# Optimization experiments

Measured on AMD Instinct MI355X. Metric: run time of the kernel, lower is better.

Reference implementation:

```python
import jax, jax.numpy as jnp
import numpy as np

N_NODES = 100000
N_EDGES = 1600000
D = 64
H = 128
EPS = 0.0  # learn_eps=False


def setup_inputs() -> dict:
    key = jax.random.key(0)
    k1, k2, k3, k4 = jax.random.split(key, 4)
    x = jax.random.normal(k1, (N_NODES, D), dtype=jnp.float32)
    edge_index = jax.random.randint(k2, (2, N_EDGES), 0, N_NODES, dtype=jnp.int64)
    W1 = jax.random.normal(k3, (D, H), dtype=jnp.float32) * (1.0 / np.sqrt(D))
    b1 = jnp.zeros((H,), dtype=jnp.float32)
    W2 = jax.random.normal(k4, (H, D), dtype=jnp.float32) * (1.0 / np.sqrt(H))
    b2 = jnp.zeros((D,), dtype=jnp.float32)
    return {"x": x, "edge_index": edge_index, "W1": W1, "b1": b1, "W2": W2, "b2": b2}


def reference(x, edge_index, W1, b1, W2, b2):
    src, dst = edge_index[0], edge_index[1]
    # gather neighbor features and scatter-add to destination nodes
    agg = jax.ops.segment_sum(x[src], dst, num_segments=N_NODES)  # [N, D]
    out = agg + (1.0 + EPS) * x
    # GIN MLP: Linear -> ReLU -> Linear
    h = jax.nn.relu(out @ W1 + b1)
    return h @ W2 + b2
```

## Files before the change

kernel.cpp:

```cpp
#include <hip/hip_runtime.h>

#define N_NODES 100000
#define N_EDGES 1600000
#define D 64
#define H 128
#define SCAN_BS 512
#define SCAN_NBLK ((N_NODES + SCAN_BS - 1) / SCAN_BS)

#define NB 1563
#define NCHUNK 256
#define EPC (N_EDGES / NCHUNK)
#define BCAP 2560
#define OVF_CAP 4096

#define MFMA_GRID 768
#define SH_STRIDE 132
#define SH16_ST 136

typedef __attribute__((ext_vector_type(8))) short short8;
typedef __attribute__((ext_vector_type(4))) float floatx4;
typedef __attribute__((ext_vector_type(4))) unsigned short ushort4_t;
typedef __attribute__((ext_vector_type(8))) unsigned short ushort8_t;

__device__ __forceinline__ unsigned short f2bf(float f) {
    unsigned u = __builtin_bit_cast(unsigned, f);
    u += 0x7FFFu + ((u >> 16) & 1u);
    return (unsigned short)(u >> 16);
}
__device__ __forceinline__ float bf2f(unsigned short u) {
    unsigned v = ((unsigned)u) << 16;
    return __builtin_bit_cast(float, v);
}

__global__ __launch_bounds__(256) void k_zero(int* __restrict__ p, int n) {
    int i = blockIdx.x * 256 + threadIdx.x;
    if (i < n) p[i] = 0;
}

__global__ __launch_bounds__(256) void k_pre(const float4* __restrict__ x4,
                                             ushort4_t* __restrict__ y, int n4,
                                             const int* __restrict__ dst,
                                             int* __restrict__ M2,
                                             int* __restrict__ ovfn,
                                             const float* __restrict__ W1,
                                             const float* __restrict__ W2,
                                             unsigned short* __restrict__ gW1b,
                                             unsigned short* __restrict__ gW2b) {
    __shared__ int hist[NB];
    int t = threadIdx.x, blk = blockIdx.x;
    if (blk < NCHUNK) {
        int c = blk;
        if (c == 0 && t == 0) ovfn[0] = 0;
        for (int i = t; i < NB; i += 256) hist[i] = 0;
        __syncthreads();
        const int* dp = dst + c * EPC;
        for (int i = t; i < EPC; i += 256) atomicAdd(&hist[dp[i] >> 6], 1);
        __syncthreads();
        int* mp = M2 + c * NB;
        for (int i = t; i < NB; i += 256) mp[i] = hist[i];
    } else if (blk == NCHUNK) {
        for (int q = t; q < 8192; q += 256) {
            int j = q & 7, l = (q >> 3) & 63, f = q >> 9;
            int nt = f & 7, kt = f >> 3;
            int k = kt * 32 + ((l >> 4) << 3) + j;
            int n = nt * 16 + (l & 15);
            gW1b[q] = f2bf(W1[k * H + n]);
        }
    } else if (blk == NCHUNK + 1) {
        for (int q = t; q < 8192; q += 256) {
            int j = q & 7, l = (q >> 3) & 63, f = q >> 9;
            int nt = f & 3, kt = f >> 2;
            int k = kt * 32 + ((l >> 4) << 3) + j;
            int n = nt * 16 + (l & 15);
            gW2b[q] = f2bf(W2[k * D + n]);
        }
    } else {
        int cb = blk - NCHUNK - 2;
        int nconv = gridDim.x - NCHUNK - 2;
        for (int i = cb * 256 + t; i < n4; i += nconv * 256) {
            float4 v = x4[i];
            ushort4_t o;
            o[0] = f2bf(v.x); o[1] = f2bf(v.y); o[2] = f2bf(v.z); o[3] = f2bf(v.w);
            y[i] = o;
        }
    }
}

__global__ __launch_bounds__(256) void k_colscan(int* __restrict__ M2,
                                                 int* __restrict__ colsum) {
    int b = blockIdx.x * 256 + threadIdx.x;
    if (b >= NB) return;
    int run = 0;
    for (int c = 0; c < NCHUNK; c++) {
        int v = M2[c * NB + b];
        M2[c * NB + b] = run;
        run += v;
    }
    colsum[b] = run;
}

__global__ __launch_bounds__(512) void k_bscan(const int* __restrict__ colsum,
                                               int* __restrict__ bends) {
    __shared__ int part[512];
    int t = threadIdx.x;
    int i0 = t * 4;
    int v0 = (i0 + 0 < NB) ? colsum[i0 + 0] : 0;
    int v1 = (i0 + 1 < NB) ? colsum[i0 + 1] : 0;
    int v2 = (i0 + 2 < NB) ? colsum[i0 + 2] : 0;
    int v3 = (i0 + 3 < NB) ? colsum[i0 + 3] : 0;
    int r0 = v0, r1 = r0 + v1, r2 = r1 + v2, r3 = r2 + v3;
    part[t] = r3;
    __syncthreads();
    for (int off = 1; off < 512; off <<= 1) {
        int u = (t >= off) ? part[t - off] : 0;
        __syncthreads();
        part[t] += u;
        __syncthreads();
    }
    int base = (t > 0) ? part[t - 1] : 0;
    if (i0 + 0 < NB) bends[i0 + 0] = base + r0;
    if (i0 + 1 < NB) bends[i0 + 1] = base + r1;
    if (i0 + 2 < NB) bends[i0 + 2] = base + r2;
    if (i0 + 3 < NB) bends[i0 + 3] = base + r3;
}

__global__ __launch_bounds__(256) void k_part(const int* __restrict__ src,
                                              const int* __restrict__ dst,
                                              const int* __restrict__ M2,
                                              const int* __restrict__ bends,
                                              int* __restrict__ ebuf) {
    __shared__ int cur[NB];
    int t = threadIdx.x, c = blockIdx.x;
    const int* mp = M2 + c * NB;
    for (int i = t; i < NB; i += 256)
        cur[i] = ((i > 0) ? bends[i - 1] : 0) + mp[i];
    __syncthreads();
    const int* sp = src + c * EPC;
    const int* dp = dst + c * EPC;
    for (int i = t; i < EPC; i += 256) {
        int d = dp[i], s = sp[i];
        int p = atomicAdd(&cur[d >> 6], 1);
        ebuf[p] = s | ((d & 63) << 17);
    }
}

__global__ __launch_bounds__(256) void k_bagg4(const float* __restrict__ x,
                                               const unsigned short* __restrict__ x16,
                                               const int* __restrict__ ebuf,
                                               const int* __restrict__ bends,
                                               int* __restrict__ ovfn,
                                               int* __restrict__ ovf,
                                               unsigned short* __restrict__ o16) {
    __shared__ int scur[64];
    __shared__ int snd[64];
    __shared__ int slist[BCAP];
    int t = threadIdx.x, b = blockIdx.x;
    int estart = (b > 0) ? bends[b - 1] : 0;
    int ne = bends[b] - estart;
    const int* ep = ebuf + estart;

    if (t < 64) scur[t] = 0;
    __syncthreads();
    for (int i = t; i < ne; i += 256) atomicAdd(&scur[ep[i] >> 17], 1);
    __syncthreads();
    if (t < 64) {
        int v = scur[t], s = v;
#pragma unroll
        for (int off = 1; off < 64; off <<= 1) {
            int u = __shfl_up(s, off, 64);
            if (t >= off) s += u;
        }
        snd[t] = s;
        scur[t] = s - v;
    }
    __syncthreads();
    for (int i = t; i < ne; i += 256) {
        int v = ep[i];
        int p = atomicAdd(&scur[v >> 17], 1);
        if (p < BCAP) {
            slist[p] = v & 0x1FFFF;
        } else {
            int o = atomicAdd(ovfn, 1);
            if (o < OVF_CAP) { ovf[2 * o] = b * 64 + (v >> 17); ovf[2 * o + 1] = v & 0x1FFFF; }
        }
    }
    __syncthreads();

    int g = t >> 3;
    int l8 = t & 7;
#pragma unroll
    for (int k = 0; k < 2; k++) {
        int dlow = g * 2 + k;
        int node = b * 64 + dlow;
        int s0 = (dlow > 0) ? snd[dlow - 1] : 0;
        int e1 = snd[dlow];
        if (s0 > BCAP) s0 = BCAP;
        if (e1 > BCAP) e1 = BCAP;
        float accA[8], accB[8];
#pragma unroll
        for (int j = 0; j < 8; j++) { accA[j] = 0.f; accB[j] = 0.f; }
        int i = s0;
        for (; i + 4 <= e1; i += 4) {
            int sA = slist[i], sB = slist[i + 1], sC = slist[i + 2], sD = slist[i + 3];
            ushort8_t uA = *(const ushort8_t*)&x16[(size_t)sA * D + l8 * 8];
            ushort8_t uB = *(const ushort8_t*)&x16[(size_t)sB * D + l8 * 8];
            ushort8_t uC = *(const ushort8_t*)&x16[(size_t)sC * D + l8 * 8];
            ushort8_t uD = *(const ushort8_t*)&x16[(size_t)sD * D + l8 * 8];
#pragma unroll
            for (int j = 0; j < 8; j++) accA[j] += bf2f(uA[j]);
#pragma unroll
            for (int j = 0; j < 8; j++) accB[j] += bf2f(uB[j]);
#pragma unroll
            for (int j = 0; j < 8; j++) accA[j] += bf2f(uC[j]);
#pragma unroll
            for (int j = 0; j < 8; j++) accB[j] += bf2f(uD[j]);
        }
        for (; i < e1; i++) {
            int sA = slist[i];
            ushort8_t uA = *(const ushort8_t*)&x16[(size_t)sA * D + l8 * 8];
#pragma unroll
            for (int j = 0; j < 8; j++) accA[j] += bf2f(uA[j]);
        }
        if (node < N_NODES) {
            const float* xp = x + (size_t)node * D + l8 * 8;
            float4 x0 = *(const float4*)xp;
            float4 x1 = *(const float4*)(xp + 4);
            ushort8_t o;
            o[0] = f2bf(accA[0] + accB[0] + x0.x);
            o[1] = f2bf(accA[1] + accB[1] + x0.y);
            o[2] = f2bf(accA[2] + accB[2] + x0.z);
            o[3] = f2bf(accA[3] + accB[3] + x0.w);
            o[4] = f2bf(accA[4] + accB[4] + x1.x);
            o[5] = f2bf(accA[5] + accB[5] + x1.y);
            o[6] = f2bf(accA[6] + accB[6] + x1.z);
            o[7] = f2bf(accA[7] + accB[7] + x1.w);
            *(ushort8_t*)&o16[(size_t)node * D + l8 * 8] = o;
        }
    }
}

__global__ __launch_bounds__(64) void k_ovf(const int* __restrict__ ovfn,
                                            const int* __restrict__ ovf,
                                            const float* __restrict__ x,
                                            unsigned short* __restrict__ o16) {
    int n = *ovfn;
    if (n > OVF_CAP) n = OVF_CAP;
    int f = threadIdx.x;
    for (int idx = 0; idx < n; idx++) {
        int d = ovf[2 * idx], s = ovf[2 * idx + 1];
        unsigned short* p = &o16[(size_t)d * D + f];
        *p = f2bf(bf2f(*p) + x[(size_t)s * D + f]);
    }
}

__global__ __launch_bounds__(256) void k_mlp16(const unsigned short* __restrict__ in16,
                                               float* __restrict__ outp,
                                               const unsigned short* __restrict__ gW1b,
                                               const unsigned short* __restrict__ gW2b,
                                               const float* __restrict__ b1,
                                               const float* __restrict__ b2) {
    __shared__ unsigned short sW1b[8192];
    __shared__ unsigned short sW2b[8192];
    __shared__ unsigned short sh16[4][16 * SH16_ST];
    __shared__ float sb1[H];
    __shared__ float sb2[D];

    int t = threadIdx.x;
    for (int q = t; q < 1024; q += 256) {
        *(short8*)&sW1b[q * 8] = *(const short8*)&gW1b[q * 8];
        *(short8*)&sW2b[q * 8] = *(const short8*)&gW2b[q * 8];
    }
    if (t < H) sb1[t] = b1[t];
    if (t >= H && t < H + D) sb2[t - H] = b2[t - H];
    __syncthreads();

    int w = t >> 6, l = t & 63;
    int m = l & 15, q4 = l >> 4;
    unsigned short* shw = sh16[w];

    const int NT16 = N_NODES / 16;
    const int WAVES = MFMA_GRID * 4;
    const int ITERS = (NT16 + WAVES - 1) / WAVES;

    for (int it = 0; it < ITERS; ++it) {
        int tl = it * WAVES + blockIdx.x * 4 + w;
        bool valid = tl < NT16;
        int nbase = tl * 16;

        if (valid) {
            const unsigned short* xr = in16 + (size_t)(nbase + m) * D + q4 * 8;
            short8 A0 = *(const short8*)(xr);
            short8 A1 = *(const short8*)(xr + 32);

#pragma unroll
            for (int nt = 0; nt < 8; nt++) {
                float bv = sb1[nt * 16 + m];
                floatx4 acc = {bv, bv, bv, bv};
                short8 B0 = *(const short8*)&sW1b[(0 * 8 + nt) * 512 + l * 8];
                short8 B1 = *(const short8*)&sW1b[(1 * 8 + nt) * 512 + l * 8];
                acc = __builtin_amdgcn_mfma_f32_16x16x32_bf16(A0, B0, acc, 0, 0, 0);
                acc = __builtin_amdgcn_mfma_f32_16x16x32_bf16(A1, B1, acc, 0, 0, 0);
#pragma unroll
                for (int r = 0; r < 4; r++)
                    shw[(q4 * 4 + r) * SH16_ST + nt * 16 + m] = f2bf(fmaxf(acc[r], 0.f));
            }
        }
        __syncthreads();

        if (valid) {
            short8 Ah[4];
#pragma unroll
            for (int kt = 0; kt < 4; kt++)
                Ah[kt] = *(const short8*)&shw[m * SH16_ST + kt * 32 + q4 * 8];
#pragma unroll
            for (int nt = 0; nt < 4; nt++) {
                float bv = sb2[nt * 16 + m];
                floatx4 acc = {bv, bv, bv, bv};
#pragma unroll
                for (int kt = 0; kt < 4; kt++) {
                    short8 B = *(const short8*)&sW2b[(kt * 4 + nt) * 512 + l * 8];
                    acc = __builtin_amdgcn_mfma_f32_16x16x32_bf16(Ah[kt], B, acc, 0, 0, 0);
                }
#pragma unroll
                for (int r = 0; r < 4; r++)
                    outp[(size_t)(nbase + q4 * 4 + r) * D + nt * 16 + m] = acc[r];
            }
        }
        __syncthreads();
    }
}

__global__ __launch_bounds__(256) void k_mlp_f32(float* __restrict__ io,
                                                 const float* __restrict__ W1,
                                                 const float* __restrict__ b1,
                                                 const float* __restrict__ W2,
                                                 const float* __restrict__ b2) {
    __shared__ unsigned short sW1b[8192];
    __shared__ unsigned short sW2b[8192];
    __shared__ float sh[4][16 * SH_STRIDE];
    __shared__ float sb1[H];
    __shared__ float sb2[D];

    int t = threadIdx.x;

    for (int q = t; q < 8192; q += 256) {
        int j = q & 7, l = (q >> 3) & 63, f = q >> 9;
        int nt = f & 7, kt = f >> 3;
        int k = kt * 32 + ((l >> 4) << 3) + j;
        int n = nt * 16 + (l & 15);
        sW1b[q] = f2bf(W1[k * H + n]);
    }
    for (int q = t; q < 8192; q += 256) {
        int j = q & 7, l = (q >> 3) & 63, f = q >> 9;
        int nt = f & 3, kt = f >> 2;
        int k = kt * 32 + ((l >> 4) << 3) + j;
        int n = nt * 16 + (l & 15);
        sW2b[q] = f2bf(W2[k * D + n]);
    }
    if (t < H) sb1[t] = b1[t];
    if (t >= H && t < H + D) sb2[t - H] = b2[t - H];
    __syncthreads();

    int w = t >> 6, l = t & 63;
    int m = l & 15, q4 = l >> 4;
    float* shw = sh[w];

    const int NT16 = N_NODES / 16;
    const int WAVES = 512 * 4;
    const int ITERS = (NT16 + WAVES - 1) / WAVES;

    for (int it = 0; it < ITERS; ++it) {
        int tl = it * WAVES + blockIdx.x * 4 + w;
        bool valid = tl < NT16;
        int nbase = tl * 16;

        if (valid) {
            const float* xr = io + (size_t)(nbase + m) * D + q4 * 8;
            float4 a0 = *(const float4*)(xr);
            float4 a1 = *(const float4*)(xr + 4);
            float4 c0 = *(const float4*)(xr + 32);
            float4 c1 = *(const float4*)(xr + 36);
            short8 A0, A1;
            A0[0] = f2bf(a0.x); A0[1] = f2bf(a0.y); A0[2] = f2bf(a0.z); A0[3] = f2bf(a0.w);
            A0[4] = f2bf(a1.x); A0[5] = f2bf(a1.y); A0[6] = f2bf(a1.z); A0[7] = f2bf(a1.w);
            A1[0] = f2bf(c0.x); A1[1] = f2bf(c0.y); A1[2] = f2bf(c0.z); A1[3] = f2bf(c0.w);
            A1[4] = f2bf(c1.x); A1[5] = f2bf(c1.y); A1[6] = f2bf(c1.z); A1[7] = f2bf(c1.w);

#pragma unroll
            for (int nt = 0; nt < 8; nt++) {
                float bv = sb1[nt * 16 + m];
                floatx4 acc = {bv, bv, bv, bv};
                short8 B0 = *(const short8*)&sW1b[(0 * 8 + nt) * 512 + l * 8];
                short8 B1 = *(const short8*)&sW1b[(1 * 8 + nt) * 512 + l * 8];
                acc = __builtin_amdgcn_mfma_f32_16x16x32_bf16(A0, B0, acc, 0, 0, 0);
                acc = __builtin_amdgcn_mfma_f32_16x16x32_bf16(A1, B1, acc, 0, 0, 0);
#pragma unroll
                for (int r = 0; r < 4; r++)
                    shw[(q4 * 4 + r) * SH_STRIDE + nt * 16 + m] = fmaxf(acc[r], 0.f);
            }
        }
        __syncthreads();

        if (valid) {
            short8 Ah[4];
#pragma unroll
            for (int kt = 0; kt < 4; kt++) {
                const float* hr = &shw[m * SH_STRIDE + kt * 32 + q4 * 8];
                float4 h0 = *(const float4*)(hr);
                float4 h1 = *(const float4*)(hr + 4);
                Ah[kt][0] = f2bf(h0.x); Ah[kt][1] = f2bf(h0.y);
                Ah[kt][2] = f2bf(h0.z); Ah[kt][3] = f2bf(h0.w);
                Ah[kt][4] = f2bf(h1.x); Ah[kt][5] = f2bf(h1.y);
                Ah[kt][6] = f2bf(h1.z); Ah[kt][7] = f2bf(h1.w);
            }
#pragma unroll
            for (int nt = 0; nt < 4; nt++) {
                float bv = sb2[nt * 16 + m];
                floatx4 acc = {bv, bv, bv, bv};
#pragma unroll
                for (int kt = 0; kt < 4; kt++) {
                    short8 B = *(const short8*)&sW2b[(kt * 4 + nt) * 512 + l * 8];
                    acc = __builtin_amdgcn_mfma_f32_16x16x32_bf16(Ah[kt], B, acc, 0, 0, 0);
                }
#pragma unroll
                for (int r = 0; r < 4; r++)
                    io[(size_t)(nbase + q4 * 4 + r) * D + nt * 16 + m] = acc[r];
            }
        }
        __syncthreads();
    }
}

__global__ __launch_bounds__(SCAN_BS) void k_scan1(const int* __restrict__ cnt,
                                                   int* __restrict__ ends,
                                                   int* __restrict__ bsum, int n) {
    __shared__ int s[SCAN_BS];
    int t = threadIdx.x, b = blockIdx.x;
    int id = b * SCAN_BS + t;
    s[t] = (id < n) ? cnt[id] : 0;
    __syncthreads();
    for (int off = 1; off < SCAN_BS; off <<= 1) {
        int u = (t >= off) ? s[t - off] : 0;
        __syncthreads();
        s[t] += u;
        __syncthreads();
    }
    if (id < n) ends[id] = s[t];
    if (t == SCAN_BS - 1) bsum[b] = s[t];
}

__global__ __launch_bounds__(256) void k_scan2(int* __restrict__ bsum, int nb) {
    __shared__ int s[256];
    int t = threadIdx.x;
    s[t] = (t < nb) ? bsum[t] : 0;
    __syncthreads();
    for (int off = 1; off < 256; off <<= 1) {
        int u = (t >= off) ? s[t - off] : 0;
        __syncthreads();
        s[t] += u;
        __syncthreads();
    }
    if (t < nb) bsum[t] = s[t];
}

__global__ __launch_bounds__(SCAN_BS) void k_scan3(int* __restrict__ ends,
                                                   const int* __restrict__ bsum, int n) {
    int t = threadIdx.x, b = blockIdx.x;
    int id = b * SCAN_BS + t;
    if (b > 0 && id < n) ends[id] += bsum[b - 1];
}

__global__ __launch_bounds__(256) void k_histpos(const int* __restrict__ dst,
                                                 int* __restrict__ cnt,
                                                 int* __restrict__ pos) {
    int e = blockIdx.x * 256 + threadIdx.x;
    if (e < N_EDGES) pos[e] = atomicAdd(&cnt[dst[e]], 1);
}

__global__ __launch_bounds__(256) void k_fill2(const int* __restrict__ src,
                                               const int* __restrict__ dst,
                                               const int* __restrict__ pos,
                                               const int* __restrict__ ends,
                                               int* __restrict__ csr) {
    int e = blockIdx.x * 256 + threadIdx.x;
    if (e >= N_EDGES) return;
    int d = dst[e];
    int start = (d > 0) ? ends[d - 1] : 0;
    csr[start + pos[e]] = src[e];
}

__global__ __launch_bounds__(256) void k_agg(const float* __restrict__ x,
                                             const int* __restrict__ csr,
                                             const int* __restrict__ ends,
                                             float* __restrict__ out) {
    int node = blockIdx.x * 4 + (threadIdx.x >> 6);
    if (node >= N_NODES) return;
    int f = threadIdx.x & 63;
    int start = (node > 0) ? ends[node - 1] : 0;
    int end = ends[node];
    float a0 = x[(size_t)node * D + f], a1 = 0.f, a2 = 0.f, a3 = 0.f;
    int e = start;
    for (; e + 4 <= end; e += 4) {
        int s0 = csr[e], s1 = csr[e + 1], s2 = csr[e + 2], s3 = csr[e + 3];
        a0 += x[(size_t)s0 * D + f];
        a1 += x[(size_t)s1 * D + f];
        a2 += x[(size_t)s2 * D + f];
        a3 += x[(size_t)s3 * D + f];
    }
    for (; e < end; e++) a0 += x[(size_t)csr[e] * D + f];
    out[(size_t)node * D + f] = (a0 + a1) + (a2 + a3);
}

__global__ __launch_bounds__(256) void k_init(const float4* __restrict__ x4,
                                              float4* __restrict__ agg4, int n4) {
    int i = blockIdx.x * 256 + threadIdx.x;
    if (i < n4) agg4[i] = x4[i];
}

__global__ __launch_bounds__(256) void k_scatter(const float4* __restrict__ x4,
                                                 const int* __restrict__ src,
                                                 const int* __restrict__ dst,
                                                 float* __restrict__ agg) {
    int gid = blockIdx.x * 256 + threadIdx.x;
    int e = gid >> 4;
    if (e >= N_EDGES) return;
    int c = gid & 15;
    float4 v = x4[src[e] * 16 + c];
    float* p = agg + (size_t)dst[e] * D + c * 4;
    atomicAdd(p + 0, v.x);
    atomicAdd(p + 1, v.y);
    atomicAdd(p + 2, v.z);
    atomicAdd(p + 3, v.w);
}

extern "C" void kernel_launch(void* const* d_in, const int* in_sizes, int n_in,
                              void* d_out, int out_size, void* d_ws, size_t ws_size,
                              hipStream_t stream) {
    const float* x  = (const float*)d_in[0];
    const int* eidx = (const int*)d_in[1];
    const float* W1 = (const float*)d_in[2];
    const float* b1 = (const float*)d_in[3];
    const float* W2 = (const float*)d_in[4];
    const float* b2 = (const float*)d_in[5];
    float* out      = (float*)d_out;

    const int* src = eidx;
    const int* dst = eidx + N_EDGES;

    int ge = (N_EDGES + 255) / 256;
    int n4 = N_NODES * D / 4;

    size_t need_A = (size_t)N_NODES * D * 2 * sizeof(unsigned short)
                  + (size_t)(N_EDGES + NCHUNK * NB + 2 * NB + 4 + 2 * OVF_CAP) * sizeof(int)
                  + (size_t)16384 * sizeof(unsigned short);
    size_t need_B = (size_t)(2 * N_NODES + 512 + 2 * N_EDGES) * sizeof(int);

    if (ws_size >= need_A) {
        unsigned short* x16 = (unsigned short*)d_ws;
        unsigned short* o16 = x16 + (size_t)N_NODES * D;
        int* ebuf   = (int*)(o16 + (size_t)N_NODES * D);
        int* M2     = ebuf + N_EDGES;
        int* colsum = M2 + NCHUNK * NB;
        int* bends  = colsum + NB;
        int* ovfn   = bends + NB;
        int* ovf    = ovfn + 4;
        unsigned short* gW1b = (unsigned short*)(ovf + 2 * OVF_CAP);
        unsigned short* gW2b = gW1b + 8192;

        k_pre<<<NCHUNK + 2 + 2048, 256, 0, stream>>>((const float4*)x, (ushort4_t*)x16, n4,
                                                     dst, M2, ovfn, W1, W2, gW1b, gW2b);
        k_colscan<<<(NB + 255) / 256, 256, 0, stream>>>(M2, colsum);
        k_bscan<<<1, 512, 0, stream>>>(colsum, bends);
        k_part<<<NCHUNK, 256, 0, stream>>>(src, dst, M2, bends, ebuf);
        k_bagg4<<<NB, 256, 0, stream>>>(x, x16, ebuf, bends, ovfn, ovf, o16);
        k_ovf<<<1, 64, 0, stream>>>(ovfn, ovf, x, o16);
        k_mlp16<<<MFMA_GRID, 256, 0, stream>>>(o16, out, gW1b, gW2b, b1, b2);
    } else if (ws_size >= need_B) {
        int* cnt  = (int*)d_ws;
        int* ends = cnt + N_NODES;
        int* bsum = ends + N_NODES;
        int* pos  = bsum + 512;
        int* csr  = pos + N_EDGES;

        k_zero<<<(N_NODES + 255) / 256, 256, 0, stream>>>(cnt, N_NODES);
        k_histpos<<<ge, 256, 0, stream>>>(dst, cnt, pos);
        k_scan1<<<SCAN_NBLK, SCAN_BS, 0, stream>>>(cnt, ends, bsum, N_NODES);
        k_scan2<<<1, 256, 0, stream>>>(bsum, SCAN_NBLK);
        k_scan3<<<SCAN_NBLK, SCAN_BS, 0, stream>>>(ends, bsum, N_NODES);
        k_fill2<<<ge, 256, 0, stream>>>(src, dst, pos, ends, csr);
        k_agg<<<(N_NODES + 3) / 4, 256, 0, stream>>>(x, csr, ends, out);
        k_mlp_f32<<<512, 256, 0, stream>>>(out, W1, b1, W2, b2);
    } else {
        k_init<<<(n4 + 255) / 256, 256, 0, stream>>>((const float4*)x, (float4*)out, n4);
        long long total = (long long)N_EDGES * 16;
        k_scatter<<<(int)((total + 255) / 256), 256, 0, stream>>>(
            (const float4*)x, src, dst, out);
        k_mlp_f32<<<512, 256, 0, stream>>>(out, W1, b1, W2, b2);
    }
}
```

Baseline: 176.9 us.

## Merge graph preprocessing into one cooperative kernel with global-atomic partitioning

Replaces the chunked histogram, column scan, block scan, partition and bucket-aggregate kernels with a single cooperative kernel that uses grid.sync between phases. It uses global atomics for a 32-node bucket histogram and partition cursors, and every block redundantly scans the bucket histogram in shared memory. Oversized buckets are handled by tiling the edge list instead of an overflow path. The goal is to remove several launches and the per-chunk count matrix. The cost is heavy global atomic contention, grid-wide barriers, and a partition order that is no longer deterministic.

```diff
diff --git a/kernel.cpp b/kernel.cpp
--- a/kernel.cpp
+++ b/kernel.cpp
@@ -1,4 +1,7 @@
 #include <hip/hip_runtime.h>
+#include <hip/hip_cooperative_groups.h>
+
+namespace cg = cooperative_groups;
 
 #define N_NODES 100000
 #define N_EDGES 1600000
@@ -7,11 +10,9 @@
 #define SCAN_BS 512
 #define SCAN_NBLK ((N_NODES + SCAN_BS - 1) / SCAN_BS)
 
-#define NB 1563
-#define NCHUNK 256
-#define EPC (N_EDGES / NCHUNK)
-#define BCAP 2560
-#define OVF_CAP 4096
+#define BK 32
+#define NB2 3125
+#define BCAP2 1536
 
 #define MFMA_GRID 768
 #define SH_STRIDE 132
@@ -32,33 +33,31 @@
     return __builtin_bit_cast(float, v);
 }
 
-__global__ __launch_bounds__(256) void k_zero(int* __restrict__ p, int n) {
-    int i = blockIdx.x * 256 + threadIdx.x;
-    if (i < n) p[i] = 0;
-}
-
-__global__ __launch_bounds__(256) void k_pre(const float4* __restrict__ x4,
-                                             ushort4_t* __restrict__ y, int n4,
-                                             const int* __restrict__ dst,
-                                             int* __restrict__ M2,
-                                             int* __restrict__ ovfn,
-                                             const float* __restrict__ W1,
-                                             const float* __restrict__ W2,
-                                             unsigned short* __restrict__ gW1b,
-                                             unsigned short* __restrict__ gW2b) {
-    __shared__ int hist[NB];
-    int t = threadIdx.x, blk = blockIdx.x;
-    if (blk < NCHUNK) {
-        int c = blk;
-        if (c == 0 && t == 0) ovfn[0] = 0;
-        for (int i = t; i < NB; i += 256) hist[i] = 0;
-        __syncthreads();
-        const int* dp = dst + c * EPC;
-        for (int i = t; i < EPC; i += 256) atomicAdd(&hist[dp[i] >> 6], 1);
-        __syncthreads();
-        int* mp = M2 + c * NB;
-        for (int i = t; i < NB; i += 256) mp[i] = hist[i];
-    } else if (blk == NCHUNK) {
+
+__device__ __forceinline__ void phase_pre(const float* x, unsigned short* x16,
+                                          const int* dst,
+                                          const float* W1, const float* W2,
+                                          unsigned short* gW1b,
+                                          unsigned short* gW2b,
+                                          int* bhist) {
+    int t = threadIdx.x;
+    int stride = gridDim.x * 256;
+    int start = blockIdx.x * 256 + t;
+
+    for (int i = start; i < N_EDGES; i += stride)
+        atomicAdd(&bhist[dst[i] >> 5], 1);
+
+    const float4* x4 = (const float4*)x;
+    ushort4_t* y = (ushort4_t*)x16;
+    const int n4 = N_NODES * D / 4;
+    for (int i = start; i < n4; i += stride) {
+        float4 v = x4[i];
+        ushort4_t o;
+        o[0] = f2bf(v.x); o[1] = f2bf(v.y); o[2] = f2bf(v.z); o[3] = f2bf(v.w);
+        y[i] = o;
+    }
+
+    if (blockIdx.x == 0) {
         for (int q = t; q < 8192; q += 256) {
             int j = q & 7, l = (q >> 3) & 63, f = q >> 9;
             int nt = f & 7, kt = f >> 3;
@@ -66,7 +65,7 @@
             int n = nt * 16 + (l & 15);
             gW1b[q] = f2bf(W1[k * H + n]);
         }
-    } else if (blk == NCHUNK + 1) {
+    } else if (blockIdx.x == 1) {
         for (int q = t; q < 8192; q += 256) {
             int j = q & 7, l = (q >> 3) & 63, f = q >> 9;
             int nt = f & 3, kt = f >> 2;
@@ -74,183 +73,187 @@
             int n = nt * 16 + (l & 15);
             gW2b[q] = f2bf(W2[k * D + n]);
         }
-    } else {
-        int cb = blk - NCHUNK - 2;
-        int nconv = gridDim.x - NCHUNK - 2;
-        for (int i = cb * 256 + t; i < n4; i += nconv * 256) {
-            float4 v = x4[i];
-            ushort4_t o;
-            o[0] = f2bf(v.x); o[1] = f2bf(v.y); o[2] = f2bf(v.z); o[3] = f2bf(v.w);
-            y[i] = o;
-        }
-    }
-}
-
-__global__ __launch_bounds__(256) void k_colscan(int* __restrict__ M2,
-                                                 int* __restrict__ colsum) {
-    int b = blockIdx.x * 256 + threadIdx.x;
-    if (b >= NB) return;
-    int run = 0;
-    for (int c = 0; c < NCHUNK; c++) {
-        int v = M2[c * NB + b];
-        M2[c * NB + b] = run;
-        run += v;
-    }
-    colsum[b] = run;
-}
-
-__global__ __launch_bounds__(512) void k_bscan(const int* __restrict__ colsum,
-                                               int* __restrict__ bends) {
-    __shared__ int part[512];
+    }
+}
+
+__device__ __forceinline__ void phase_scan(const int* bhist, int* sstart,
+                                           int* spart) {
     int t = threadIdx.x;
-    int i0 = t * 4;
-    int v0 = (i0 + 0 < NB) ? colsum[i0 + 0] : 0;
-    int v1 = (i0 + 1 < NB) ? colsum[i0 + 1] : 0;
-    int v2 = (i0 + 2 < NB) ? colsum[i0 + 2] : 0;
-    int v3 = (i0 + 3 < NB) ? colsum[i0 + 3] : 0;
-    int r0 = v0, r1 = r0 + v1, r2 = r1 + v2, r3 = r2 + v3;
-    part[t] = r3;
+    int base = t * 13;
+    int v[13];
+    int s = 0;
+#pragma unroll
+    for (int j = 0; j < 13; j++) {
+        int idx = base + j;
+        v[j] = (idx < NB2) ? bhist[idx] : 0;
+        s += v[j];
+    }
+    spart[t] = s;
     __syncthreads();
-    for (int off = 1; off < 512; off <<= 1) {
-        int u = (t >= off) ? part[t - off] : 0;
-        __syncthreads();
-        part[t] += u;
-        __syncthreads();
-    }
-    int base = (t > 0) ? part[t - 1] : 0;
-    if (i0 + 0 < NB) bends[i0 + 0] = base + r0;
-    if (i0 + 1 < NB) bends[i0 + 1] = base + r1;
-    if (i0 + 2 < NB) bends[i0 + 2] = base + r2;
-    if (i0 + 3 < NB) bends[i0 + 3] = base + r3;
-}
-
-__global__ __launch_bounds__(256) void k_part(const int* __restrict__ src,
-                                              const int* __restrict__ dst,
-                                              const int* __restrict__ M2,
-                                              const int* __restrict__ bends,
-                                              int* __restrict__ ebuf) {
-    __shared__ int cur[NB];
-    int t = threadIdx.x, c = blockIdx.x;
-    const int* mp = M2 + c * NB;
-    for (int i = t; i < NB; i += 256)
-        cur[i] = ((i > 0) ? bends[i - 1] : 0) + mp[i];
+    for (int off = 1; off < 256; off <<= 1) {
+        int u = (t >= off) ? spart[t - off] : 0;
+        __syncthreads();
+        spart[t] += u;
+        __syncthreads();
+    }
+    int run = (t > 0) ? spart[t - 1] : 0;
+#pragma unroll
+    for (int j = 0; j < 13; j++) {
+        int idx = base + j;
+        if (idx < NB2) sstart[idx] = run;
+        run += v[j];
+    }
+    if (t == 0) sstart[NB2] = N_EDGES;
     __syncthreads();
-    const int* sp = src + c * EPC;
-    const int* dp = dst + c * EPC;
-    for (int i = t; i < EPC; i += 256) {
-        int d = dp[i], s = sp[i];
-        int p = atomicAdd(&cur[d >> 6], 1);
-        ebuf[p] = s | ((d & 63) << 17);
-    }
-}
-
-__global__ __launch_bounds__(256) void k_bagg4(const float* __restrict__ x,
-                                               const unsigned short* __restrict__ x16,
-                                               const int* __restrict__ ebuf,
-                                               const int* __restrict__ bends,
-                                               int* __restrict__ ovfn,
-                                               int* __restrict__ ovf,
-                                               unsigned short* __restrict__ o16) {
-    __shared__ int scur[64];
-    __shared__ int snd[64];
-    __shared__ int slist[BCAP];
-    int t = threadIdx.x, b = blockIdx.x;
-    int estart = (b > 0) ? bends[b - 1] : 0;
-    int ne = bends[b] - estart;
-    const int* ep = ebuf + estart;
-
-    if (t < 64) scur[t] = 0;
-    __syncthreads();
-    for (int i = t; i < ne; i += 256) atomicAdd(&scur[ep[i] >> 17], 1);
-    __syncthreads();
-    if (t < 64) {
-        int v = scur[t], s = v;
-#pragma unroll
-        for (int off = 1; off < 64; off <<= 1) {
-            int u = __shfl_up(s, off, 64);
-            if (t >= off) s += u;
-        }
-        snd[t] = s;
-        scur[t] = s - v;
-    }
-    __syncthreads();
-    for (int i = t; i < ne; i += 256) {
-        int v = ep[i];
-        int p = atomicAdd(&scur[v >> 17], 1);
-        if (p < BCAP) {
-            slist[p] = v & 0x1FFFF;
-        } else {
-            int o = atomicAdd(ovfn, 1);
-            if (o < OVF_CAP) { ovf[2 * o] = b * 64 + (v >> 17); ovf[2 * o + 1] = v & 0x1FFFF; }
-        }
-    }
-    __syncthreads();
-
+}
+
+__device__ __forceinline__ void phase_part(const int* src, const int* dst,
+                                           const int* sstart, int* ccur,
+                                           int* ebuf) {
+    int t = threadIdx.x;
+    int stride = gridDim.x * 256;
+    for (int i = blockIdx.x * 256 + t; i < N_EDGES; i += stride) {
+        int d = dst[i], s = src[i];
+        int b = d >> 5;
+        int p = sstart[b] + atomicAdd(&ccur[b], 1);
+        ebuf[p] = s | ((d & 31) << 17);
+    }
+}
+
+__device__ __forceinline__ void phase_bagg(const float* x,
+                                           const unsigned short* x16,
+                                           const int* ebuf, const int* sstart,
+                                           int* scur, int* snd, int* slist,
+                                           unsigned short* o16) {
+    int t = threadIdx.x;
     int g = t >> 3;
     int l8 = t & 7;
-#pragma unroll
-    for (int k = 0; k < 2; k++) {
-        int dlow = g * 2 + k;
-        int node = b * 64 + dlow;
-        int s0 = (dlow > 0) ? snd[dlow - 1] : 0;
-        int e1 = snd[dlow];
-        if (s0 > BCAP) s0 = BCAP;
-        if (e1 > BCAP) e1 = BCAP;
+    for (int b = blockIdx.x; b < NB2; b += gridDim.x) {
+        int estart = sstart[b];
+        int ne = sstart[b + 1] - estart;
+        const int* ep = ebuf + estart;
         float accA[8], accB[8];
 #pragma unroll
         for (int j = 0; j < 8; j++) { accA[j] = 0.f; accB[j] = 0.f; }
-        int i = s0;
-        for (; i + 4 <= e1; i += 4) {
-            int sA = slist[i], sB = slist[i + 1], sC = slist[i + 2], sD = slist[i + 3];
-            ushort8_t uA = *(const ushort8_t*)&x16[(size_t)sA * D + l8 * 8];
-            ushort8_t uB = *(const ushort8_t*)&x16[(size_t)sB * D + l8 * 8];
-            ushort8_t uC = *(const ushort8_t*)&x16[(size_t)sC * D + l8 * 8];
-            ushort8_t uD = *(const ushort8_t*)&x16[(size_t)sD * D + l8 * 8];
-#pragma unroll
-            for (int j = 0; j < 8; j++) accA[j] += bf2f(uA[j]);
-#pragma unroll
-            for (int j = 0; j < 8; j++) accB[j] += bf2f(uB[j]);
-#pragma unroll
-            for (int j = 0; j < 8; j++) accA[j] += bf2f(uC[j]);
-#pragma unroll
-            for (int j = 0; j < 8; j++) accB[j] += bf2f(uD[j]);
-        }
-        for (; i < e1; i++) {
-            int sA = slist[i];
-            ushort8_t uA = *(const ushort8_t*)&x16[(size_t)sA * D + l8 * 8];
-#pragma unroll
-            for (int j = 0; j < 8; j++) accA[j] += bf2f(uA[j]);
-        }
-        if (node < N_NODES) {
-            const float* xp = x + (size_t)node * D + l8 * 8;
-            float4 x0 = *(const float4*)xp;
-            float4 x1 = *(const float4*)(xp + 4);
-            ushort8_t o;
-            o[0] = f2bf(accA[0] + accB[0] + x0.x);
-            o[1] = f2bf(accA[1] + accB[1] + x0.y);
-            o[2] = f2bf(accA[2] + accB[2] + x0.z);
-            o[3] = f2bf(accA[3] + accB[3] + x0.w);
-            o[4] = f2bf(accA[4] + accB[4] + x1.x);
-            o[5] = f2bf(accA[5] + accB[5] + x1.y);
-            o[6] = f2bf(accA[6] + accB[6] + x1.z);
-            o[7] = f2bf(accA[7] + accB[7] + x1.w);
-            *(ushort8_t*)&o16[(size_t)node * D + l8 * 8] = o;
-        }
-    }
-}
-
-__global__ __launch_bounds__(64) void k_ovf(const int* __restrict__ ovfn,
-                                            const int* __restrict__ ovf,
-                                            const float* __restrict__ x,
-                                            unsigned short* __restrict__ o16) {
-    int n = *ovfn;
-    if (n > OVF_CAP) n = OVF_CAP;
-    int f = threadIdx.x;
-    for (int idx = 0; idx < n; idx++) {
-        int d = ovf[2 * idx], s = ovf[2 * idx + 1];
-        unsigned short* p = &o16[(size_t)d * D + f];
-        *p = f2bf(bf2f(*p) + x[(size_t)s * D + f]);
-    }
+
+        int ntile = (ne + BCAP2 - 1) / BCAP2;
+        for (int T = 0; T < ntile; T++) {
+            int toff = T * BCAP2;
+            int tn = ne - toff;
+            if (tn > BCAP2) tn = BCAP2;
+            __syncthreads();
+            if (t < BK) scur[t] = 0;
+            __syncthreads();
+            for (int i = t; i < tn; i += 256)
+                atomicAdd(&scur[ep[toff + i] >> 17], 1);
+            __syncthreads();
+            if (t < BK) {
+                int v = scur[t], s = v;
+#pragma unroll
+                for (int off = 1; off < BK; off <<= 1) {
+                    int u = __shfl_up(s, off, 64);
+                    if (t >= off) s += u;
+                }
+                snd[t] = s;
+                scur[t] = s - v;
+            }
+            __syncthreads();
+            for (int i = t; i < tn; i += 256) {
+                int v = ep[toff + i];
+                int p = atomicAdd(&scur[v >> 17], 1);
+                slist[p] = v & 0x1FFFF;
+            }
+            __syncthreads();
+
+            int s0 = (g > 0) ? snd[g - 1] : 0;
+            int e1 = snd[g];
+            int i2 = s0;
+            for (; i2 + 4 <= e1; i2 += 4) {
+                int sA = slist[i2], sB = slist[i2 + 1];
+                int sC = slist[i2 + 2], sD = slist[i2 + 3];
+                ushort8_t uA = *(const ushort8_t*)&x16[(size_t)sA * D + l8 * 8];
+                ushort8_t uB = *(const ushort8_t*)&x16[(size_t)sB * D + l8 * 8];
+                ushort8_t uC = *(const ushort8_t*)&x16[(size_t)sC * D + l8 * 8];
+                ushort8_t uD = *(const ushort8_t*)&x16[(size_t)sD * D + l8 * 8];
+#pragma unroll
+                for (int j = 0; j < 8; j++) accA[j] += bf2f(uA[j]);
+#pragma unroll
+                for (int j = 0; j < 8; j++) accB[j] += bf2f(uB[j]);
+#pragma unroll
+                for (int j = 0; j < 8; j++) accA[j] += bf2f(uC[j]);
+#pragma unroll
+                for (int j = 0; j < 8; j++) accB[j] += bf2f(uD[j]);
+            }
+            for (; i2 < e1; i2++) {
+                ushort8_t uA =
+                    *(const ushort8_t*)&x16[(size_t)slist[i2] * D + l8 * 8];
+#pragma unroll
+                for (int j = 0; j < 8; j++) accA[j] += bf2f(uA[j]);
+            }
+        }
+
+        int node = b * BK + g;
+        const float* xp = x + (size_t)node * D + l8 * 8;
+        float4 x0 = *(const float4*)xp;
+        float4 x1 = *(const float4*)(xp + 4);
+        ushort8_t o;
+        o[0] = f2bf(accA[0] + accB[0] + x0.x);
+        o[1] = f2bf(accA[1] + accB[1] + x0.y);
+        o[2] = f2bf(accA[2] + accB[2] + x0.z);
+        o[3] = f2bf(accA[3] + accB[3] + x0.w);
+        o[4] = f2bf(accA[4] + accB[4] + x1.x);
+        o[5] = f2bf(accA[5] + accB[5] + x1.y);
+        o[6] = f2bf(accA[6] + accB[6] + x1.z);
+        o[7] = f2bf(accA[7] + accB[7] + x1.w);
+        *(ushort8_t*)&o16[(size_t)node * D + l8 * 8] = o;
+    }
+}
+
+__global__ __launch_bounds__(256) void k_graph(const float* x,
+                                               unsigned short* x16,
+                                               const int* src, const int* dst,
+                                               const float* W1,
+                                               const float* W2,
+                                               unsigned short* gW1b,
+                                               unsigned short* gW2b,
+                                               int* bhist, int* ccur,
+                                               int* ebuf,
+                                               unsigned short* o16) {
+    __shared__ int sstart[NB2 + 1];
+    __shared__ int sbuf[2 * BK + BCAP2];
+    cg::grid_group grid = cg::this_grid();
+
+    phase_pre(x, x16, dst, W1, W2, gW1b, gW2b, bhist);
+    grid.sync();
+    phase_scan(bhist, sstart, sbuf);
+    phase_part(src, dst, sstart, ccur, ebuf);
+    grid.sync();
+    phase_bagg(x, x16, ebuf, sstart, sbuf, sbuf + BK, sbuf + 2 * BK, o16);
+}
+
+__global__ __launch_bounds__(256) void k_p1(const float* x, unsigned short* x16,
+                                            const int* dst, const float* W1,
+                                            const float* W2,
+                                            unsigned short* gW1b,
+                                            unsigned short* gW2b, int* bhist) {
+    phase_pre(x, x16, dst, W1, W2, gW1b, gW2b, bhist);
+}
+__global__ __launch_bounds__(256) void k_p2(const int* src, const int* dst,
+                                            const int* bhist, int* ccur,
+                                            int* ebuf) {
+    __shared__ int sstart[NB2 + 1];
+    __shared__ int sbuf[2 * BK + BCAP2];
+    phase_scan(bhist, sstart, sbuf);
+    phase_part(src, dst, sstart, ccur, ebuf);
+}
+__global__ __launch_bounds__(256) void k_p3(const float* x,
+                                            const unsigned short* x16,
+                                            const int* ebuf, const int* bhist,
+                                            unsigned short* o16) {
+    __shared__ int sstart[NB2 + 1];
+    __shared__ int sbuf[2 * BK + BCAP2];
+    phase_scan(bhist, sstart, sbuf);
+    phase_bagg(x, x16, ebuf, sstart, sbuf, sbuf + BK, sbuf + 2 * BK, o16);
 }
 
 __global__ __launch_bounds__(256) void k_mlp16(const unsigned short* __restrict__ in16,
@@ -328,6 +331,11 @@
         }
         __syncthreads();
     }
+}
+
+__global__ __launch_bounds__(256) void k_zero(int* __restrict__ p, int n) {
+    int i = blockIdx.x * 256 + threadIdx.x;
+    if (i < n) p[i] = 0;
 }
 
 __global__ __launch_bounds__(256) void k_mlp_f32(float* __restrict__ io,
@@ -551,29 +559,47 @@
     int n4 = N_NODES * D / 4;
 
     size_t need_A = (size_t)N_NODES * D * 2 * sizeof(unsigned short)
-                  + (size_t)(N_EDGES + NCHUNK * NB + 2 * NB + 4 + 2 * OVF_CAP) * sizeof(int)
-                  + (size_t)16384 * sizeof(unsigned short);
+                  + (size_t)N_EDGES * sizeof(int)
+                  + (size_t)16384 * sizeof(unsigned short)
+                  + (size_t)2 * NB2 * sizeof(int);
     size_t need_B = (size_t)(2 * N_NODES + 512 + 2 * N_EDGES) * sizeof(int);
 
     if (ws_size >= need_A) {
         unsigned short* x16 = (unsigned short*)d_ws;
         unsigned short* o16 = x16 + (size_t)N_NODES * D;
         int* ebuf   = (int*)(o16 + (size_t)N_NODES * D);
-        int* M2     = ebuf + N_EDGES;
-        int* colsum = M2 + NCHUNK * NB;
-        int* bends  = colsum + NB;
-        int* ovfn   = bends + NB;
-        int* ovf    = ovfn + 4;
-        unsigned short* gW1b = (unsigned short*)(ovf + 2 * OVF_CAP);
+        unsigned short* gW1b = (unsigned short*)(ebuf + N_EDGES);
         unsigned short* gW2b = gW1b + 8192;
-
-        k_pre<<<NCHUNK + 2 + 2048, 256, 0, stream>>>((const float4*)x, (ushort4_t*)x16, n4,
-                                                     dst, M2, ovfn, W1, W2, gW1b, gW2b);
-        k_colscan<<<(NB + 255) / 256, 256, 0, stream>>>(M2, colsum);
-        k_bscan<<<1, 512, 0, stream>>>(colsum, bends);
-        k_part<<<NCHUNK, 256, 0, stream>>>(src, dst, M2, bends, ebuf);
-        k_bagg4<<<NB, 256, 0, stream>>>(x, x16, ebuf, bends, ovfn, ovf, o16);
-        k_ovf<<<1, 64, 0, stream>>>(ovfn, ovf, x, o16);
+        int* bhist  = (int*)(gW2b + 8192);
+        int* ccur   = bhist + NB2;
+
+        static int G = 0;
+        if (G == 0) {
+            int nb = 0;
+            if (hipOccupancyMaxActiveBlocksPerMultiprocessor(&nb, k_graph, 256, 0)
+                    != hipSuccess || nb < 1)
+                nb = 1;
+            long g = (long)nb * 256;
+            if (g > 1024) g = 1024;
+            if (g < 256) g = 256;
+            G = (int)g;
+        }
+
+        hipMemsetAsync(bhist, 0, 2 * NB2 * sizeof(int), stream);
+
+        const float* xa = x;
+        unsigned short* x16a = x16;
+        void* kargs[] = {(void*)&xa, (void*)&x16a, (void*)&src, (void*)&dst,
+                         (void*)&W1, (void*)&W2, (void*)&gW1b, (void*)&gW2b,
+                         (void*)&bhist, (void*)&ccur, (void*)&ebuf, (void*)&o16};
+        hipError_t ce = hipLaunchCooperativeKernel(k_graph, dim3(G), dim3(256),
+                                                   kargs, 0u, stream);
+        if (ce != hipSuccess) {
+            (void)hipGetLastError();
+            k_p1<<<1024, 256, 0, stream>>>(x, x16, dst, W1, W2, gW1b, gW2b, bhist);
+            k_p2<<<1024, 256, 0, stream>>>(src, dst, bhist, ccur, ebuf);
+            k_p3<<<1024, 256, 0, stream>>>(x, x16, ebuf, bhist, o16);
+        }
         k_mlp16<<<MFMA_GRID, 256, 0, stream>>>(o16, out, gW1b, gW2b, b1, b2);
     } else if (ws_size >= need_B) {
         int* cnt  = (int*)d_ws;
```

Result: slower. 622.5 us (+251.9%).

## Fold bucket scan into partition kernel and tile aggregation to drop overflow path

Applied to the files above, without the earlier changes.

The single-block bucket-end scan is recomputed redundantly inside every partition block, which removes one kernel launch. The overflow buffer and its serial fix-up kernel are replaced by processing each bucket's edges in tiles of BCAP, with accumulators kept in registers across tiles. The gather inner loop unroll drops from 4 to 2 loads per iteration across two register accumulator sets. The trade-offs are redundant scan work in every block, lower memory-level parallelism in the gather, and higher register pressure.

```diff
diff --git a/kernel.cpp b/kernel.cpp
--- a/kernel.cpp
+++ b/kernel.cpp
@@ -11,7 +11,6 @@
 #define NCHUNK 256
 #define EPC (N_EDGES / NCHUNK)
 #define BCAP 2560
-#define OVF_CAP 4096
 
 #define MFMA_GRID 768
 #define SH_STRIDE 132
@@ -32,16 +31,10 @@
     return __builtin_bit_cast(float, v);
 }
 
-__global__ __launch_bounds__(256) void k_zero(int* __restrict__ p, int n) {
-    int i = blockIdx.x * 256 + threadIdx.x;
-    if (i < n) p[i] = 0;
-}
-
 __global__ __launch_bounds__(256) void k_pre(const float4* __restrict__ x4,
                                              ushort4_t* __restrict__ y, int n4,
                                              const int* __restrict__ dst,
                                              int* __restrict__ M2,
-                                             int* __restrict__ ovfn,
                                              const float* __restrict__ W1,
                                              const float* __restrict__ W2,
                                              unsigned short* __restrict__ gW1b,
@@ -50,7 +43,6 @@
     int t = threadIdx.x, blk = blockIdx.x;
     if (blk < NCHUNK) {
         int c = blk;
-        if (c == 0 && t == 0) ovfn[0] = 0;
         for (int i = t; i < NB; i += 256) hist[i] = 0;
         __syncthreads();
         const int* dp = dst + c * EPC;
@@ -99,157 +91,168 @@
     colsum[b] = run;
 }
 
-__global__ __launch_bounds__(512) void k_bscan(const int* __restrict__ colsum,
-                                               int* __restrict__ bends) {
-    __shared__ int part[512];
-    int t = threadIdx.x;
-    int i0 = t * 4;
-    int v0 = (i0 + 0 < NB) ? colsum[i0 + 0] : 0;
-    int v1 = (i0 + 1 < NB) ? colsum[i0 + 1] : 0;
-    int v2 = (i0 + 2 < NB) ? colsum[i0 + 2] : 0;
-    int v3 = (i0 + 3 < NB) ? colsum[i0 + 3] : 0;
-    int r0 = v0, r1 = r0 + v1, r2 = r1 + v2, r3 = r2 + v3;
-    part[t] = r3;
+__global__ __launch_bounds__(256) void k_part2(const int* __restrict__ src,
+                                               const int* __restrict__ dst,
+                                               const int* __restrict__ M2,
+                                               const int* __restrict__ colsum,
+                                               int* __restrict__ ebuf,
+                                               int* __restrict__ gbends) {
+    __shared__ int cur[NB];
+    __shared__ int sbends[NB];
+    __shared__ int spart[256];
+    int t = threadIdx.x, c = blockIdx.x;
+
+    int base = t * 7;
+    int v[7];
+    int s = 0;
+#pragma unroll
+    for (int j = 0; j < 7; j++) {
+        int idx = base + j;
+        v[j] = (idx < NB) ? colsum[idx] : 0;
+        s += v[j];
+    }
+    spart[t] = s;
     __syncthreads();
-    for (int off = 1; off < 512; off <<= 1) {
-        int u = (t >= off) ? part[t - off] : 0;
-        __syncthreads();
-        part[t] += u;
-        __syncthreads();
-    }
-    int base = (t > 0) ? part[t - 1] : 0;
-    if (i0 + 0 < NB) bends[i0 + 0] = base + r0;
-    if (i0 + 1 < NB) bends[i0 + 1] = base + r1;
-    if (i0 + 2 < NB) bends[i0 + 2] = base + r2;
-    if (i0 + 3 < NB) bends[i0 + 3] = base + r3;
-}
-
-__global__ __launch_bounds__(256) void k_part(const int* __restrict__ src,
-                                              const int* __restrict__ dst,
-                                              const int* __restrict__ M2,
-                                              const int* __restrict__ bends,
-                                              int* __restrict__ ebuf) {
-    __shared__ int cur[NB];
-    int t = threadIdx.x, c = blockIdx.x;
+    for (int off = 1; off < 256; off <<= 1) {
+        int u = (t >= off) ? spart[t - off] : 0;
+        __syncthreads();
+        spart[t] += u;
+        __syncthreads();
+    }
+    int run = (t > 0) ? spart[t - 1] : 0;
+#pragma unroll
+    for (int j = 0; j < 7; j++) {
+        int idx = base + j;
+        run += v[j];
+        if (idx < NB) sbends[idx] = run;
+    }
+    __syncthreads();
+
     const int* mp = M2 + c * NB;
     for (int i = t; i < NB; i += 256)
-        cur[i] = ((i > 0) ? bends[i - 1] : 0) + mp[i];
+        cur[i] = ((i > 0) ? sbends[i - 1] : 0) + mp[i];
+    if (c == 0)
+        for (int i = t; i < NB; i += 256) gbends[i] = sbends[i];
     __syncthreads();
+
     const int* sp = src + c * EPC;
     const int* dp = dst + c * EPC;
     for (int i = t; i < EPC; i += 256) {
-        int d = dp[i], s = sp[i];
+        int d = dp[i], srcv = sp[i];
         int p = atomicAdd(&cur[d >> 6], 1);
-        ebuf[p] = s | ((d & 63) << 17);
-    }
-}
-
-__global__ __launch_bounds__(256) void k_bagg4(const float* __restrict__ x,
+        ebuf[p] = srcv | ((d & 63) << 17);
+    }
+}
+
+__global__ __launch_bounds__(256) void k_bagg5(const float* __restrict__ x,
                                                const unsigned short* __restrict__ x16,
                                                const int* __restrict__ ebuf,
-                                               const int* __restrict__ bends,
-                                               int* __restrict__ ovfn,
-                                               int* __restrict__ ovf,
+                                               const int* __restrict__ gbends,
                                                unsigned short* __restrict__ o16) {
     __shared__ int scur[64];
     __shared__ int snd[64];
     __shared__ int slist[BCAP];
     int t = threadIdx.x, b = blockIdx.x;
-    int estart = (b > 0) ? bends[b - 1] : 0;
-    int ne = bends[b] - estart;
+    int estart = (b > 0) ? gbends[b - 1] : 0;
+    int ne = gbends[b] - estart;
     const int* ep = ebuf + estart;
-
-    if (t < 64) scur[t] = 0;
-    __syncthreads();
-    for (int i = t; i < ne; i += 256) atomicAdd(&scur[ep[i] >> 17], 1);
-    __syncthreads();
-    if (t < 64) {
-        int v = scur[t], s = v;
-#pragma unroll
-        for (int off = 1; off < 64; off <<= 1) {
-            int u = __shfl_up(s, off, 64);
-            if (t >= off) s += u;
-        }
-        snd[t] = s;
-        scur[t] = s - v;
-    }
-    __syncthreads();
-    for (int i = t; i < ne; i += 256) {
-        int v = ep[i];
-        int p = atomicAdd(&scur[v >> 17], 1);
-        if (p < BCAP) {
-            slist[p] = v & 0x1FFFF;
-        } else {
-            int o = atomicAdd(ovfn, 1);
-            if (o < OVF_CAP) { ovf[2 * o] = b * 64 + (v >> 17); ovf[2 * o + 1] = v & 0x1FFFF; }
-        }
-    }
-    __syncthreads();
 
     int g = t >> 3;
     int l8 = t & 7;
+    float aA0[8], aB0[8], aA1[8], aB1[8];
+#pragma unroll
+    for (int j = 0; j < 8; j++) { aA0[j] = 0.f; aB0[j] = 0.f; aA1[j] = 0.f; aB1[j] = 0.f; }
+
+    int ntile = (ne + BCAP - 1) / BCAP;
+    for (int T = 0; T < ntile; T++) {
+        int toff = T * BCAP;
+        int tn = ne - toff;
+        if (tn > BCAP) tn = BCAP;
+        __syncthreads();
+        if (t < 64) scur[t] = 0;
+        __syncthreads();
+        for (int i = t; i < tn; i += 256) atomicAdd(&scur[ep[toff + i] >> 17], 1);
+        __syncthreads();
+        if (t < 64) {
+            int v = scur[t], s = v;
+#pragma unroll
+            for (int off = 1; off < 64; off <<= 1) {
+                int u = __shfl_up(s, off, 64);
+                if (t >= off) s += u;
+            }
+            snd[t] = s;
+            scur[t] = s - v;
+        }
+        __syncthreads();
+        for (int i = t; i < tn; i += 256) {
+            int v = ep[toff + i];
+            int p = atomicAdd(&scur[v >> 17], 1);
+            slist[p] = v & 0x1FFFF;
+        }
+        __syncthreads();
+
+        {
+            int dlow = g * 2;
+            int s0 = (dlow > 0) ? snd[dlow - 1] : 0;
+            int e1 = snd[dlow];
+            int i2 = s0;
+            for (; i2 + 2 <= e1; i2 += 2) {
+                int sA = slist[i2], sB = slist[i2 + 1];
+                ushort8_t uA = *(const ushort8_t*)&x16[(size_t)sA * D + l8 * 8];
+                ushort8_t uB = *(const ushort8_t*)&x16[(size_t)sB * D + l8 * 8];
+#pragma unroll
+                for (int j = 0; j < 8; j++) aA0[j] += bf2f(uA[j]);
+#pragma unroll
+                for (int j = 0; j < 8; j++) aB0[j] += bf2f(uB[j]);
+            }
+            for (; i2 < e1; i2++) {
+                ushort8_t uA = *(const ushort8_t*)&x16[(size_t)slist[i2] * D + l8 * 8];
+#pragma unroll
+                for (int j = 0; j < 8; j++) aA0[j] += bf2f(uA[j]);
+            }
+        }
+        {
+            int dlow = g * 2 + 1;
+            int s0 = snd[dlow - 1];
+            int e1 = snd[dlow];
+            int i2 = s0;
+            for (; i2 + 2 <= e1; i2 += 2) {
+                int sA = slist[i2], sB = slist[i2 + 1];
+                ushort8_t uA = *(const ushort8_t*)&x16[(size_t)sA * D + l8 * 8];
+                ushort8_t uB = *(const ushort8_t*)&x16[(size_t)sB * D + l8 * 8];
+#pragma unroll
+                for (int j = 0; j < 8; j++) aA1[j] += bf2f(uA[j]);
+#pragma unroll
+                for (int j = 0; j < 8; j++) aB1[j] += bf2f(uB[j]);
+            }
+            for (; i2 < e1; i2++) {
+                ushort8_t uA = *(const ushort8_t*)&x16[(size_t)slist[i2] * D + l8 * 8];
+#pragma unroll
+                for (int j = 0; j < 8; j++) aA1[j] += bf2f(uA[j]);
+            }
+        }
+    }
+
 #pragma unroll
     for (int k = 0; k < 2; k++) {
-        int dlow = g * 2 + k;
-        int node = b * 64 + dlow;
-        int s0 = (dlow > 0) ? snd[dlow - 1] : 0;
-        int e1 = snd[dlow];
-        if (s0 > BCAP) s0 = BCAP;
-        if (e1 > BCAP) e1 = BCAP;
-        float accA[8], accB[8];
-#pragma unroll
-        for (int j = 0; j < 8; j++) { accA[j] = 0.f; accB[j] = 0.f; }
-        int i = s0;
-        for (; i + 4 <= e1; i += 4) {
-            int sA = slist[i], sB = slist[i + 1], sC = slist[i + 2], sD = slist[i + 3];
-            ushort8_t uA = *(const ushort8_t*)&x16[(size_t)sA * D + l8 * 8];
-            ushort8_t uB = *(const ushort8_t*)&x16[(size_t)sB * D + l8 * 8];
-            ushort8_t uC = *(const ushort8_t*)&x16[(size_t)sC * D + l8 * 8];
-            ushort8_t uD = *(const ushort8_t*)&x16[(size_t)sD * D + l8 * 8];
-#pragma unroll
-            for (int j = 0; j < 8; j++) accA[j] += bf2f(uA[j]);
-#pragma unroll
-            for (int j = 0; j < 8; j++) accB[j] += bf2f(uB[j]);
-#pragma unroll
-            for (int j = 0; j < 8; j++) accA[j] += bf2f(uC[j]);
-#pragma unroll
-            for (int j = 0; j < 8; j++) accB[j] += bf2f(uD[j]);
-        }
-        for (; i < e1; i++) {
-            int sA = slist[i];
-            ushort8_t uA = *(const ushort8_t*)&x16[(size_t)sA * D + l8 * 8];
-#pragma unroll
-            for (int j = 0; j < 8; j++) accA[j] += bf2f(uA[j]);
-        }
+        int node = b * 64 + g * 2 + k;
         if (node < N_NODES) {
             const float* xp = x + (size_t)node * D + l8 * 8;
             float4 x0 = *(const float4*)xp;
             float4 x1 = *(const float4*)(xp + 4);
+            float* pa = (k == 0) ? aA0 : aA1;
+            float* pb = (k == 0) ? aB0 : aB1;
             ushort8_t o;
-            o[0] = f2bf(accA[0] + accB[0] + x0.x);
-            o[1] = f2bf(accA[1] + accB[1] + x0.y);
-            o[2] = f2bf(accA[2] + accB[2] + x0.z);
-            o[3] = f2bf(accA[3] + accB[3] + x0.w);
-            o[4] = f2bf(accA[4] + accB[4] + x1.x);
-            o[5] = f2bf(accA[5] + accB[5] + x1.y);
-            o[6] = f2bf(accA[6] + accB[6] + x1.z);
-            o[7] = f2bf(accA[7] + accB[7] + x1.w);
+            o[0] = f2bf(pa[0] + pb[0] + x0.x);
+            o[1] = f2bf(pa[1] + pb[1] + x0.y);
+            o[2] = f2bf(pa[2] + pb[2] + x0.z);
+            o[3] = f2bf(pa[3] + pb[3] + x0.w);
+            o[4] = f2bf(pa[4] + pb[4] + x1.x);
+            o[5] = f2bf(pa[5] + pb[5] + x1.y);
+            o[6] = f2bf(pa[6] + pb[6] + x1.z);
+            o[7] = f2bf(pa[7] + pb[7] + x1.w);
             *(ushort8_t*)&o16[(size_t)node * D + l8 * 8] = o;
         }
-    }
-}
-
-__global__ __launch_bounds__(64) void k_ovf(const int* __restrict__ ovfn,
-                                            const int* __restrict__ ovf,
-                                            const float* __restrict__ x,
-                                            unsigned short* __restrict__ o16) {
-    int n = *ovfn;
-    if (n > OVF_CAP) n = OVF_CAP;
-    int f = threadIdx.x;
-    for (int idx = 0; idx < n; idx++) {
-        int d = ovf[2 * idx], s = ovf[2 * idx + 1];
-        unsigned short* p = &o16[(size_t)d * D + f];
-        *p = f2bf(bf2f(*p) + x[(size_t)s * D + f]);
     }
 }
 
@@ -328,6 +331,11 @@
         }
         __syncthreads();
     }
+}
+
+__global__ __launch_bounds__(256) void k_zero(int* __restrict__ p, int n) {
+    int i = blockIdx.x * 256 + threadIdx.x;
+    if (i < n) p[i] = 0;
 }
 
 __global__ __launch_bounds__(256) void k_mlp_f32(float* __restrict__ io,
@@ -551,29 +559,26 @@
     int n4 = N_NODES * D / 4;
 
     size_t need_A = (size_t)N_NODES * D * 2 * sizeof(unsigned short)
-                  + (size_t)(N_EDGES + NCHUNK * NB + 2 * NB + 4 + 2 * OVF_CAP) * sizeof(int)
-                  + (size_t)16384 * sizeof(unsigned short);
+                  + (size_t)N_EDGES * sizeof(int)
+                  + (size_t)16384 * sizeof(unsigned short)
+                  + (size_t)(NCHUNK * NB + 2 * NB) * sizeof(int);
     size_t need_B = (size_t)(2 * N_NODES + 512 + 2 * N_EDGES) * sizeof(int);
 
     if (ws_size >= need_A) {
         unsigned short* x16 = (unsigned short*)d_ws;
         unsigned short* o16 = x16 + (size_t)N_NODES * D;
         int* ebuf   = (int*)(o16 + (size_t)N_NODES * D);
-        int* M2     = ebuf + N_EDGES;
+        unsigned short* gW1b = (unsigned short*)(ebuf + N_EDGES);
+        unsigned short* gW2b = gW1b + 8192;
+        int* M2     = (int*)(gW2b + 8192);
         int* colsum = M2 + NCHUNK * NB;
-        int* bends  = colsum + NB;
-        int* ovfn   = bends + NB;
-        int* ovf    = ovfn + 4;
-        unsigned short* gW1b = (unsigned short*)(ovf + 2 * OVF_CAP);
-        unsigned short* gW2b = gW1b + 8192;
-
-        k_pre<<<NCHUNK + 2 + 2048, 256, 0, stream>>>((const float4*)x, (ushort4_t*)x16, n4,
-                                                     dst, M2, ovfn, W1, W2, gW1b, gW2b);
+        int* gbends = colsum + NB;
+
+        k_pre<<<NCHUNK + 2 + 2048, 256, 0, stream>>>((const float4*)x, (ushort4_t*)x16,
+                                                     n4, dst, M2, W1, W2, gW1b, gW2b);
         k_colscan<<<(NB + 255) / 256, 256, 0, stream>>>(M2, colsum);
-        k_bscan<<<1, 512, 0, stream>>>(colsum, bends);
-        k_part<<<NCHUNK, 256, 0, stream>>>(src, dst, M2, bends, ebuf);
-        k_bagg4<<<NB, 256, 0, stream>>>(x, x16, ebuf, bends, ovfn, ovf, o16);
-        k_ovf<<<1, 64, 0, stream>>>(ovfn, ovf, x, o16);
+        k_part2<<<NCHUNK, 256, 0, stream>>>(src, dst, M2, colsum, ebuf, gbends);
+        k_bagg5<<<NB, 256, 0, stream>>>(x, x16, ebuf, gbends, o16);
         k_mlp16<<<MFMA_GRID, 256, 0, stream>>>(o16, out, gW1b, gW2b, b1, b2);
     } else if (ws_size >= need_B) {
         int* cnt  = (int*)d_ws;
```

Result: no change. 173.7 us (median of 2 runs) (-1.8%).
